# Optimization experiments

Hardware: AMD Instinct MI355X
Metric: run time of the kernel (lower is better)

## Reference

```python
import jax, jax.numpy as jnp
import numpy as np

B, T, C, H = 2, 2048, 1024, 16  # batch, seq, d_model, heads
D = C // H                       # head dim = 64


def setup_inputs() -> dict:
    key = jax.random.key(0)
    ks = jax.random.split(key, 5)
    s = 0.02  # init scale for weights
    return {
        "x": jax.random.normal(ks[0], (B, T, C), jnp.float32),
        "Wq": jax.random.normal(ks[1], (C, C), jnp.float32) * s,
        "bq": jnp.zeros((C,), jnp.float32),
        "Wk": jax.random.normal(ks[2], (C, C), jnp.float32) * s,
        "bk": jnp.zeros((C,), jnp.float32),
        "Wv": jax.random.normal(ks[3], (C, C), jnp.float32) * s,
        "bv": jnp.zeros((C,), jnp.float32),
        "Wo": jax.random.normal(ks[4], (C, C), jnp.float32) * s,
        "bo": jnp.zeros((C,), jnp.float32),
    }


def reference(x, Wq, bq, Wk, bk, Wv, bv, Wo, bo):
    b, t, c = x.shape
    h, d = H, C // H
    # QKV projections (torch Linear: x @ W.T + b), split into heads: b h t d
    q = (x @ Wq.T + bq).reshape(b, t, h, d).transpose(0, 2, 1, 3)
    k = (x @ Wk.T + bk).reshape(b, t, h, d).transpose(0, 2, 1, 3)
    v = (x @ Wv.T + bv).reshape(b, t, h, d).transpose(0, 2, 1, 3)

    scale = 1.0 / float(np.sqrt(d))
    att = jnp.einsum("bhqd,bhkd->bhqk", q, k) * scale  # [B,H,T,T]
    causal = jnp.tril(jnp.ones((t, t), dtype=bool))
    att = jnp.where(causal[None, None, :, :], att, -jnp.inf)
    att = jax.nn.softmax(att, axis=-1)
    att_weights = att  # attn_dropout with p=0 is identity

    y = jnp.einsum("bhqk,bhkd->bhqd", att, v)          # [B,H,T,D]
    y = y.transpose(0, 2, 1, 3).reshape(b, t, c)        # b q (h d)
    y = y @ Wo.T + bo                                   # out proj; resid_dropout p=0
    return y, att_weights
```

## Files before the change

kernel.cpp:

```cpp
#include <hip/hip_runtime.h>

#define DI __device__ __forceinline__

typedef __attribute__((ext_vector_type(8))) short short8;
typedef __attribute__((ext_vector_type(4))) float floatx4;
typedef unsigned short u16;

#define Bb 2
#define Tt 2048
#define Cc 1024
#define Hh 16
#define Dd 64
#define C1 0.1803368801111244f
#define NEGBIG (-1e30f)

DI float bf2f(u16 u) { union { unsigned int i; float f; } v; v.i = ((unsigned int)u) << 16; return v.f; }
DI u16 f2bf(float f) {
  union { float f; unsigned int i; } v; v.f = f;
  unsigned int i = v.i;
  unsigned int r = i + 0x7fffu + ((i >> 16) & 1u);
  return (u16)(r >> 16);
}

DI floatx4 mfma16(short8 a, short8 b, floatx4 c) {
  return __builtin_amdgcn_mfma_f32_16x16x32_bf16(a, b, c, 0, 0, 0);
}

DI void gload16(const u16* g, u16* l) {
  __builtin_amdgcn_global_load_lds(
      (const __attribute__((address_space(1))) unsigned int*)(g),
      (__attribute__((address_space(3))) unsigned int*)(l), 16, 0, 0);
}

DI uint4 load8(const void* p, size_t eoff, int isbf) {
  if (isbf) {
    return *(const uint4*)((const u16*)p + eoff);
  } else {
    const float* f = (const float*)p + eoff;
    float4 a = *(const float4*)f;
    float4 b = *(const float4*)(f + 4);
    union { uint4 u; u16 s[8]; } r;
    r.s[0] = f2bf(a.x); r.s[1] = f2bf(a.y); r.s[2] = f2bf(a.z); r.s[3] = f2bf(a.w);
    r.s[4] = f2bf(b.x); r.s[5] = f2bf(b.y); r.s[6] = f2bf(b.z); r.s[7] = f2bf(b.w);
    return r.u;
  }
}

DI float loadb(const void* p, int i, int isbf) {
  return isbf ? bf2f(((const u16*)p)[i]) : ((const float*)p)[i];
}

__global__ void detect_dtype(const u16* __restrict__ x, int* __restrict__ flag) {
  __shared__ int cnt[256];
  int c = 0;
  for (int i = threadIdx.x; i < 4096; i += 256) {
    unsigned u = x[2 * i];
    unsigned e = (u >> 7) & 0xFFu;
    c += (e == 0u || (e >= 100u && e <= 150u)) ? 1 : 0;
  }
  cnt[threadIdx.x] = c;
  __syncthreads();
  for (int s = 128; s > 0; s >>= 1) {
    if ((int)threadIdx.x < s) cnt[threadIdx.x] += cnt[threadIdx.x + s];
    __syncthreads();
  }
  if (threadIdx.x == 0) *flag = (cnt[0] > 2458) ? 1 : 0;
}

__global__ __launch_bounds__(256) void convert_all(
    const void* __restrict__ x,
    const void* __restrict__ wq, const void* __restrict__ wk,
    const void* __restrict__ wv, const void* __restrict__ wo,
    u16* __restrict__ xb,
    u16* __restrict__ wqb, u16* __restrict__ wkb,
    u16* __restrict__ wvb, u16* __restrict__ wob,
    const int* __restrict__ flagp) {
  const int isbf = *flagp;
  const void* src;
  u16* dst;
  size_t n;
  switch (blockIdx.y) {
    case 0: src = x;  dst = xb;  n = (size_t)Bb * Tt * Cc; break;
    case 1: src = wq; dst = wqb; n = (size_t)Cc * Cc; break;
    case 2: src = wk; dst = wkb; n = (size_t)Cc * Cc; break;
    case 3: src = wv; dst = wvb; n = (size_t)Cc * Cc; break;
    default: src = wo; dst = wob; n = (size_t)Cc * Cc; break;
  }
  size_t i8 = ((size_t)blockIdx.x * 256 + threadIdx.x) * 8;
  size_t step = (size_t)gridDim.x * 256 * 8;
  for (; i8 < n; i8 += step) {
    uint4 v = load8(src, i8, isbf);
    *(uint4*)(dst + i8) = v;
  }
}

__global__ __launch_bounds__(256) void qkv_gemm(
    const u16* __restrict__ Xb,
    const u16* __restrict__ Wqb, const u16* __restrict__ Wkb, const u16* __restrict__ Wvb,
    const void* __restrict__ bq, const void* __restrict__ bk, const void* __restrict__ bv,
    u16* __restrict__ Qb, u16* __restrict__ Kb, u16* __restrict__ Vb,
    const int* __restrict__ flagp) {
  __shared__ __align__(16) u16 As[128 * 32];
  __shared__ __align__(16) u16 Bs[128 * 32];
  const int isbf = *flagp;
  const int z = blockIdx.z;
  const u16* W = (z == 0) ? Wqb : (z == 1) ? Wkb : Wvb;
  const void* bias = (z == 0) ? bq : (z == 1) ? bk : bv;
  u16* Out = (z == 0) ? Qb : (z == 1) ? Kb : Vb;

  const int m0 = blockIdx.y * 128, n0 = blockIdx.x * 128;
  const int tid = threadIdx.x;
  const int w = tid >> 6, lane = tid & 63, quad = lane >> 4, l15 = lane & 15;
  const int wm = w >> 1, wn = w & 1;

  floatx4 acc[4][4];
#pragma unroll
  for (int a = 0; a < 4; ++a)
#pragma unroll
    for (int b2 = 0; b2 < 4; ++b2) acc[a][b2] = (floatx4){0.f, 0.f, 0.f, 0.f};

  const int s0 = w * 128 + lane, s1 = s0 + 64;
  const int rA0 = s0 >> 2, c0 = (s0 & 3) * 8;
  const int rA1 = s1 >> 2, c1 = (s1 & 3) * 8;
  const u16* gA0 = Xb + (size_t)(m0 + rA0) * Cc + c0;
  const u16* gA1 = Xb + (size_t)(m0 + rA1) * Cc + c1;
  const u16* gB0 = W + (size_t)(n0 + rA0) * Cc + c0;
  const u16* gB1 = W + (size_t)(n0 + rA1) * Cc + c1;
  u16* lA0 = As + w * 1024;
  u16* lA1 = As + w * 1024 + 512;
  u16* lB0 = Bs + w * 1024;
  u16* lB1 = Bs + w * 1024 + 512;

  for (int k0 = 0; k0 < Cc; k0 += 32) {
    __syncthreads();
    gload16(gA0 + k0, lA0);
    gload16(gA1 + k0, lA1);
    gload16(gB0 + k0, lB0);
    gload16(gB1 + k0, lB1);
    __syncthreads();
    short8 af[4], bfv[4];
#pragma unroll
    for (int t = 0; t < 4; ++t)
      af[t] = *(const short8*)(As + (wm * 64 + t * 16 + l15) * 32 + quad * 8);
#pragma unroll
    for (int t = 0; t < 4; ++t)
      bfv[t] = *(const short8*)(Bs + (wn * 64 + t * 16 + l15) * 32 + quad * 8);
#pragma unroll
    for (int tm = 0; tm < 4; ++tm)
#pragma unroll
      for (int tn = 0; tn < 4; ++tn) acc[tm][tn] = mfma16(af[tm], bfv[tn], acc[tm][tn]);
  }

  float bb[4];
#pragma unroll
  for (int tn = 0; tn < 4; ++tn) bb[tn] = loadb(bias, n0 + wn * 64 + tn * 16 + l15, isbf);
#pragma unroll
  for (int tm = 0; tm < 4; ++tm) {
#pragma unroll
    for (int tn = 0; tn < 4; ++tn) {
      int n = n0 + wn * 64 + tn * 16 + l15;
      int h = n >> 6, d = n & 63;
#pragma unroll
      for (int r = 0; r < 4; ++r) {
        int m = m0 + wm * 64 + tm * 16 + quad * 4 + r;
        int b = m >> 11, t = m & 2047;
        Out[(((size_t)(b * Hh + h) * Tt) + t) * Dd + d] = f2bf(acc[tm][tn][r] + bb[tn]);
      }
    }
  }
}

__global__ __launch_bounds__(256) void out_gemm(
    const u16* __restrict__ Y, const u16* __restrict__ Wob, const void* __restrict__ bo,
    float* __restrict__ Out, const int* __restrict__ flagp) {
  __shared__ __align__(16) u16 As[128 * 32];
  __shared__ __align__(16) u16 Bs[128 * 32];
  const int isbf = *flagp;
  const int m0 = blockIdx.y * 128, n0 = blockIdx.x * 128;
  const int tid = threadIdx.x;
  const int w = tid >> 6, lane = tid & 63, quad = lane >> 4, l15 = lane & 15;
  const int wm = w >> 1, wn = w & 1;

  floatx4 acc[4][4];
#pragma unroll
  for (int a = 0; a < 4; ++a)
#pragma unroll
    for (int b2 = 0; b2 < 4; ++b2) acc[a][b2] = (floatx4){0.f, 0.f, 0.f, 0.f};

  const int s0 = w * 128 + lane, s1 = s0 + 64;
  const int rA0 = s0 >> 2, c0 = (s0 & 3) * 8;
  const int rA1 = s1 >> 2, c1 = (s1 & 3) * 8;
  const u16* gA0 = Y + (size_t)(m0 + rA0) * Cc + c0;
  const u16* gA1 = Y + (size_t)(m0 + rA1) * Cc + c1;
  const u16* gB0 = Wob + (size_t)(n0 + rA0) * Cc + c0;
  const u16* gB1 = Wob + (size_t)(n0 + rA1) * Cc + c1;
  u16* lA0 = As + w * 1024;
  u16* lA1 = As + w * 1024 + 512;
  u16* lB0 = Bs + w * 1024;
  u16* lB1 = Bs + w * 1024 + 512;

  for (int k0 = 0; k0 < Cc; k0 += 32) {
    __syncthreads();
    gload16(gA0 + k0, lA0);
    gload16(gA1 + k0, lA1);
    gload16(gB0 + k0, lB0);
    gload16(gB1 + k0, lB1);
    __syncthreads();
    short8 af[4], bfv[4];
#pragma unroll
    for (int t = 0; t < 4; ++t)
      af[t] = *(const short8*)(As + (wm * 64 + t * 16 + l15) * 32 + quad * 8);
#pragma unroll
    for (int t = 0; t < 4; ++t)
      bfv[t] = *(const short8*)(Bs + (wn * 64 + t * 16 + l15) * 32 + quad * 8);
#pragma unroll
    for (int tm = 0; tm < 4; ++tm)
#pragma unroll
      for (int tn = 0; tn < 4; ++tn) acc[tm][tn] = mfma16(af[tm], bfv[tn], acc[tm][tn]);
  }

  float bb[4];
#pragma unroll
  for (int tn = 0; tn < 4; ++tn) bb[tn] = loadb(bo, n0 + wn * 64 + tn * 16 + l15, isbf);
#pragma unroll
  for (int tm = 0; tm < 4; ++tm)
#pragma unroll
    for (int tn = 0; tn < 4; ++tn) {
      int n = n0 + wn * 64 + tn * 16 + l15;
#pragma unroll
      for (int r = 0; r < 4; ++r) {
        int m = m0 + wm * 64 + tm * 16 + quad * 4 + r;
        Out[(size_t)m * Cc + n] = acc[tm][tn][r] + bb[tn];
      }
    }
}

__global__ __launch_bounds__(512) void attn_kernel(
    const u16* __restrict__ Qbuf, const u16* __restrict__ Kbuf, const u16* __restrict__ Vbuf,
    float* __restrict__ Att, u16* __restrict__ Ybuf) {
  __shared__ __align__(16) u16 Ks[128 * 72];
  __shared__ __align__(16) u16 Vts[64 * 136];
  __shared__ __align__(16) u16 Ps[8 * 16 * 40];

  const int id = blockIdx.x;
  const int qt = 15 - (id >> 5);
  const int hb = id & 31;
  const int b = hb >> 4, h = hb & 15;

  const int tid = threadIdx.x;
  const int w = tid >> 6, lane = tid & 63, quad = lane >> 4, l15 = lane & 15;

  const size_t headoff = (size_t)(b * Hh + h) * Tt * Dd;
  const u16* Qh = Qbuf + headoff;
  const u16* Kh = Kbuf + headoff;
  const u16* Vh = Vbuf + headoff;
  float* attO = Att + (size_t)(b * Hh + h) * Tt * Tt;
  u16* Psw = Ps + w * 640;

  const int q0 = qt * 128;
  const int qw = q0 + w * 16;

  const int vrow = tid >> 2, vcb = (tid & 3) * 16;

  short8 aq0 = *(const short8*)(Qh + (size_t)(qw + l15) * Dd + quad * 8);
  short8 aq1 = *(const short8*)(Qh + (size_t)(qw + l15) * Dd + 32 + quad * 8);

  float m4[4], l4[4];
#pragma unroll
  for (int r = 0; r < 4; ++r) { m4[r] = NEGBIG; l4[r] = 0.f; }

  for (int c = 0; c <= qt; ++c) {
    const int kb = c * 128;
    __syncthreads();
#pragma unroll
    for (int i = 0; i < 2; ++i) {
      int slot = tid + i * 512;
      int rr = slot >> 3, g = slot & 7;
      *(uint4*)(Ks + rr * 72 + g * 8) = *(const uint4*)(Kh + (size_t)(kb + rr) * Dd + g * 8);
    }
    __syncthreads();

    floatx4 s[8];
#pragma unroll
    for (int kt = 0; kt < 8; ++kt) {
      short8 b0 = *(const short8*)(Ks + (kt * 16 + l15) * 72 + quad * 8);
      short8 b1 = *(const short8*)(Ks + (kt * 16 + l15) * 72 + 32 + quad * 8);
      floatx4 t = (floatx4){0.f, 0.f, 0.f, 0.f};
      t = mfma16(aq0, b0, t);
      t = mfma16(aq1, b1, t);
      s[kt] = t;
    }
    const bool partial = (kb + 127 > qw);
#pragma unroll
    for (int r = 0; r < 4; ++r) {
      const int qi = qw + quad * 4 + r;
      float e[8];
      float bm = NEGBIG;
#pragma unroll
      for (int kt = 0; kt < 8; ++kt) {
        float s2 = s[kt][r] * C1;
        if (partial) {
          int key = kb + kt * 16 + l15;
          s2 = (key <= qi) ? s2 : NEGBIG;
        }
        e[kt] = s2;
        bm = fmaxf(bm, s2);
      }
      float mn = fmaxf(m4[r], bm);
      float sum = 0.f;
#pragma unroll
      for (int kt = 0; kt < 8; ++kt) sum += exp2f(e[kt] - mn);
      l4[r] = l4[r] * exp2f(m4[r] - mn) + sum;
      m4[r] = mn;
    }
  }
#pragma unroll
  for (int r = 0; r < 4; ++r) {
    float m = m4[r], l = l4[r];
#pragma unroll
    for (int off = 1; off <= 8; off <<= 1) {
      float mo = __shfl_xor(m, off, 64);
      float lo = __shfl_xor(l, off, 64);
      float mn = fmaxf(m, mo);
      l = l * exp2f(m - mn) + lo * exp2f(mo - mn);
      m = mn;
    }
    m4[r] = m; l4[r] = l;
  }
  float lrec[4];
#pragma unroll
  for (int r = 0; r < 4; ++r) lrec[r] = 1.0f / l4[r];

  floatx4 yacc[4];
#pragma unroll
  for (int dt = 0; dt < 4; ++dt) yacc[dt] = (floatx4){0.f, 0.f, 0.f, 0.f};

  uint4 va = *(const uint4*)(Vh + (size_t)vrow * Dd + vcb);
  uint4 vb = *(const uint4*)(Vh + (size_t)vrow * Dd + vcb + 8);

  for (int c = 0; c <= qt; ++c) {
    const int kb = c * 128;
    __syncthreads();
#pragma unroll
    for (int i = 0; i < 2; ++i) {
      int slot = tid + i * 512;
      int rr = slot >> 3, g = slot & 7;
      *(uint4*)(Ks + rr * 72 + g * 8) = *(const uint4*)(Kh + (size_t)(kb + rr) * Dd + g * 8);
    }
    {
      union { uint4 u; u16 sv[8]; } cv;
      cv.u = va;
#pragma unroll
      for (int j = 0; j < 8; ++j) Vts[(vcb + j) * 136 + vrow] = cv.sv[j];
      cv.u = vb;
#pragma unroll
      for (int j = 0; j < 8; ++j) Vts[(vcb + 8 + j) * 136 + vrow] = cv.sv[j];
    }
    if (c < qt) {
      va = *(const uint4*)(Vh + (size_t)(kb + 128 + vrow) * Dd + vcb);
      vb = *(const uint4*)(Vh + (size_t)(kb + 128 + vrow) * Dd + vcb + 8);
    }
    __syncthreads();

    floatx4 s[8];
#pragma unroll
    for (int kt = 0; kt < 8; ++kt) {
      short8 b0 = *(const short8*)(Ks + (kt * 16 + l15) * 72 + quad * 8);
      short8 b1 = *(const short8*)(Ks + (kt * 16 + l15) * 72 + 32 + quad * 8);
      floatx4 t = (floatx4){0.f, 0.f, 0.f, 0.f};
      t = mfma16(aq0, b0, t);
      t = mfma16(aq1, b1, t);
      s[kt] = t;
    }

    const bool partial = (kb + 127 > qw);
#pragma unroll
    for (int ks = 0; ks < 4; ++ks) {
#pragma unroll
      for (int kk = 0; kk < 2; ++kk) {
        const int kt = ks * 2 + kk;
#pragma unroll
        for (int r = 0; r < 4; ++r) {
          const int row = quad * 4 + r;
          const int qi = qw + row;
          const int key = kb + kt * 16 + l15;
          float p = exp2f(fminf(s[kt][r] * C1 - m4[r], 0.f)) * lrec[r];
          if (partial && key > qi) p = 0.f;
          attO[(size_t)qi * Tt + key] = p;
          Psw[row * 40 + kk * 16 + l15] = f2bf(p);
        }
      }
      short8 ap = *(const short8*)(Psw + l15 * 40 + quad * 8);
#pragma unroll
      for (int dt = 0; dt < 4; ++dt) {
        short8 bv = *(const short8*)(Vts + (dt * 16 + l15) * 136 + ks * 32 + quad * 8);
        yacc[dt] = mfma16(ap, bv, yacc[dt]);
      }
    }
  }

  {
    uint4 z; z.x = 0u; z.y = 0u; z.z = 0u; z.w = 0u;
    for (int c = qt + 1; c < 16; ++c) {
      const int kb = c * 128;
#pragma unroll
      for (int i = 0; i < 8; ++i) {
        int slot = tid + i * 512;
        int row = slot >> 5, g = slot & 31;
        *(uint4*)(attO + (size_t)(q0 + row) * Tt + kb + g * 4) = z;
      }
    }
  }

#pragma unroll
  for (int dt = 0; dt < 4; ++dt) {
#pragma unroll
    for (int r = 0; r < 4; ++r) {
      const int qi = qw + quad * 4 + r;
      Ybuf[(size_t)(b * Tt + qi) * Cc + h * Dd + dt * 16 + l15] = f2bf(yacc[dt][r]);
    }
  }
}

extern "C" void kernel_launch(void* const* d_in, const int* in_sizes, int n_in,
                              void* d_out, int out_size, void* d_ws, size_t ws_size,
                              hipStream_t stream) {
  const void* x  = d_in[0];
  const void* Wq = d_in[1];
  const void* bq = d_in[2];
  const void* Wk = d_in[3];
  const void* bk = d_in[4];
  const void* Wv = d_in[5];
  const void* bv = d_in[6];
  const void* Wo = d_in[7];
  const void* bo = d_in[8];
  float* out = (float*)d_out;

  const size_t NTC = (size_t)Bb * Tt * Cc;
  const size_t CC = (size_t)Cc * Cc;

  char* wsb = (char*)d_ws;
  int* flag = (int*)wsb;
  u16* Qb = (u16*)(wsb + 256);
  u16* Kb = Qb + NTC;
  u16* Vb = Kb + NTC;
  u16* Yb = Vb + NTC;
  u16* Xb = Yb + NTC;
  u16* Wqb = Xb + NTC;
  u16* Wkb = Wqb + CC;
  u16* Wvb = Wkb + CC;
  u16* Wob = Wvb + CC;

  hipLaunchKernelGGL(detect_dtype, dim3(1), dim3(256), 0, stream, (const u16*)x, flag);
  hipLaunchKernelGGL(convert_all, dim3(512, 5), dim3(256), 0, stream,
                     x, Wq, Wk, Wv, Wo, Xb, Wqb, Wkb, Wvb, Wob, flag);
  hipLaunchKernelGGL(qkv_gemm, dim3(8, 32, 3), dim3(256), 0, stream,
                     Xb, Wqb, Wkb, Wvb, bq, bk, bv, Qb, Kb, Vb, flag);
  float* attOut = out + NTC;
  hipLaunchKernelGGL(attn_kernel, dim3(512), dim3(512), 0, stream,
                     Qb, Kb, Vb, attOut, Yb);
  hipLaunchKernelGGL(out_gemm, dim3(8, 32, 1), dim3(256), 0, stream,
                     Yb, Wob, bo, out, flag);
}
```

Baseline: 706.5 us.

## Split attention into stats and PV kernels with smaller 64-row query tiles

Splits the fused two-pass attention kernel into two kernels. The first computes per-row softmax max and reciprocal sum into a workspace buffer. The second recomputes scores, writes the normalized attention probabilities and accumulates P·V. Query tiles shrink from 128 to 64 rows and blocks from 512 to 256 threads, doubling the grid for better load balance and occupancy. The cost is an extra launch, a small stats buffer round-trip, and partially wasted work on the diagonal key block, since 128-key chunks now cover 64-row tiles.

```diff
diff --git a/kernel.cpp b/kernel.cpp
--- a/kernel.cpp
+++ b/kernel.cpp
@@ -235,15 +235,13 @@
     }
 }
 
-__global__ __launch_bounds__(512) void attn_kernel(
-    const u16* __restrict__ Qbuf, const u16* __restrict__ Kbuf, const u16* __restrict__ Vbuf,
-    float* __restrict__ Att, u16* __restrict__ Ybuf) {
+__global__ __launch_bounds__(256) void attn_stats(
+    const u16* __restrict__ Qbuf, const u16* __restrict__ Kbuf,
+    float2* __restrict__ Sb) {
   __shared__ __align__(16) u16 Ks[128 * 72];
-  __shared__ __align__(16) u16 Vts[64 * 136];
-  __shared__ __align__(16) u16 Ps[8 * 16 * 40];
 
   const int id = blockIdx.x;
-  const int qt = 15 - (id >> 5);
+  const int qt = 31 - (id >> 5);
   const int hb = id & 31;
   const int b = hb >> 4, h = hb & 15;
 
@@ -253,14 +251,9 @@
   const size_t headoff = (size_t)(b * Hh + h) * Tt * Dd;
   const u16* Qh = Qbuf + headoff;
   const u16* Kh = Kbuf + headoff;
-  const u16* Vh = Vbuf + headoff;
-  float* attO = Att + (size_t)(b * Hh + h) * Tt * Tt;
-  u16* Psw = Ps + w * 640;
-
-  const int q0 = qt * 128;
+
+  const int q0 = qt * 64;
   const int qw = q0 + w * 16;
-
-  const int vrow = tid >> 2, vcb = (tid & 3) * 16;
 
   short8 aq0 = *(const short8*)(Qh + (size_t)(qw + l15) * Dd + quad * 8);
   short8 aq1 = *(const short8*)(Qh + (size_t)(qw + l15) * Dd + 32 + quad * 8);
@@ -269,12 +262,14 @@
 #pragma unroll
   for (int r = 0; r < 4; ++r) { m4[r] = NEGBIG; l4[r] = 0.f; }
 
-  for (int c = 0; c <= qt; ++c) {
+  const int nact = (qt >> 1) + 1;
+
+  for (int c = 0; c < nact; ++c) {
     const int kb = c * 128;
     __syncthreads();
 #pragma unroll
-    for (int i = 0; i < 2; ++i) {
-      int slot = tid + i * 512;
+    for (int i = 0; i < 4; ++i) {
+      int slot = tid + i * 256;
       int rr = slot >> 3, g = slot & 7;
       *(uint4*)(Ks + rr * 72 + g * 8) = *(const uint4*)(Kh + (size_t)(kb + rr) * Dd + g * 8);
     }
@@ -327,38 +322,94 @@
     }
     m4[r] = m; l4[r] = l;
   }
-  float lrec[4];
-#pragma unroll
-  for (int r = 0; r < 4; ++r) lrec[r] = 1.0f / l4[r];
+  if (l15 == 0) {
+#pragma unroll
+    for (int r = 0; r < 4; ++r) {
+      int qi = qw + quad * 4 + r;
+      float2 st; st.x = m4[r]; st.y = 1.0f / l4[r];
+      Sb[(size_t)(b * Hh + h) * Tt + qi] = st;
+    }
+  }
+}
+
+__global__ __launch_bounds__(256) void attn_pv(
+    const u16* __restrict__ Qbuf, const u16* __restrict__ Kbuf, const u16* __restrict__ Vbuf,
+    const float2* __restrict__ Sb,
+    float* __restrict__ Att, u16* __restrict__ Ybuf) {
+  __shared__ __align__(16) u16 Ks[128 * 72];
+  __shared__ __align__(16) u16 Vts[64 * 136];
+  __shared__ __align__(16) u16 Ps[4 * 16 * 40];
+
+  const int id = blockIdx.x;
+  const int qt = 31 - (id >> 5);
+  const int hb = id & 31;
+  const int b = hb >> 4, h = hb & 15;
+
+  const int tid = threadIdx.x;
+  const int w = tid >> 6, lane = tid & 63, quad = lane >> 4, l15 = lane & 15;
+
+  const size_t headoff = (size_t)(b * Hh + h) * Tt * Dd;
+  const u16* Qh = Qbuf + headoff;
+  const u16* Kh = Kbuf + headoff;
+  const u16* Vh = Vbuf + headoff;
+  float* attO = Att + (size_t)(b * Hh + h) * Tt * Tt;
+  u16* Psw = Ps + w * 640;
+
+  const int q0 = qt * 64;
+  const int qw = q0 + w * 16;
+
+  const int vrow = tid >> 1, vcb = (tid & 1) * 32;
+
+  short8 aq0 = *(const short8*)(Qh + (size_t)(qw + l15) * Dd + quad * 8);
+  short8 aq1 = *(const short8*)(Qh + (size_t)(qw + l15) * Dd + 32 + quad * 8);
+
+  float m4[4], lrec[4];
+#pragma unroll
+  for (int r = 0; r < 4; ++r) {
+    float2 st = Sb[(size_t)(b * Hh + h) * Tt + qw + quad * 4 + r];
+    m4[r] = st.x; lrec[r] = st.y;
+  }
 
   floatx4 yacc[4];
 #pragma unroll
   for (int dt = 0; dt < 4; ++dt) yacc[dt] = (floatx4){0.f, 0.f, 0.f, 0.f};
 
-  uint4 va = *(const uint4*)(Vh + (size_t)vrow * Dd + vcb);
-  uint4 vb = *(const uint4*)(Vh + (size_t)vrow * Dd + vcb + 8);
-
-  for (int c = 0; c <= qt; ++c) {
+  const int nact = (qt >> 1) + 1;
+
+  uint4 v0 = *(const uint4*)(Vh + (size_t)vrow * Dd + vcb);
+  uint4 v1 = *(const uint4*)(Vh + (size_t)vrow * Dd + vcb + 8);
+  uint4 v2 = *(const uint4*)(Vh + (size_t)vrow * Dd + vcb + 16);
+  uint4 v3 = *(const uint4*)(Vh + (size_t)vrow * Dd + vcb + 24);
+
+  for (int c = 0; c < nact; ++c) {
     const int kb = c * 128;
     __syncthreads();
 #pragma unroll
-    for (int i = 0; i < 2; ++i) {
-      int slot = tid + i * 512;
+    for (int i = 0; i < 4; ++i) {
+      int slot = tid + i * 256;
       int rr = slot >> 3, g = slot & 7;
       *(uint4*)(Ks + rr * 72 + g * 8) = *(const uint4*)(Kh + (size_t)(kb + rr) * Dd + g * 8);
     }
     {
       union { uint4 u; u16 sv[8]; } cv;
-      cv.u = va;
+      cv.u = v0;
 #pragma unroll
       for (int j = 0; j < 8; ++j) Vts[(vcb + j) * 136 + vrow] = cv.sv[j];
-      cv.u = vb;
+      cv.u = v1;
 #pragma unroll
       for (int j = 0; j < 8; ++j) Vts[(vcb + 8 + j) * 136 + vrow] = cv.sv[j];
-    }
-    if (c < qt) {
-      va = *(const uint4*)(Vh + (size_t)(kb + 128 + vrow) * Dd + vcb);
-      vb = *(const uint4*)(Vh + (size_t)(kb + 128 + vrow) * Dd + vcb + 8);
+      cv.u = v2;
+#pragma unroll
+      for (int j = 0; j < 8; ++j) Vts[(vcb + 16 + j) * 136 + vrow] = cv.sv[j];
+      cv.u = v3;
+#pragma unroll
+      for (int j = 0; j < 8; ++j) Vts[(vcb + 24 + j) * 136 + vrow] = cv.sv[j];
+    }
+    if (c + 1 < nact) {
+      v0 = *(const uint4*)(Vh + (size_t)(kb + 128 + vrow) * Dd + vcb);
+      v1 = *(const uint4*)(Vh + (size_t)(kb + 128 + vrow) * Dd + vcb + 8);
+      v2 = *(const uint4*)(Vh + (size_t)(kb + 128 + vrow) * Dd + vcb + 16);
+      v3 = *(const uint4*)(Vh + (size_t)(kb + 128 + vrow) * Dd + vcb + 24);
     }
     __syncthreads();
 
@@ -401,11 +452,11 @@
 
   {
     uint4 z; z.x = 0u; z.y = 0u; z.z = 0u; z.w = 0u;
-    for (int c = qt + 1; c < 16; ++c) {
+    for (int c = nact; c < 16; ++c) {
       const int kb = c * 128;
 #pragma unroll
       for (int i = 0; i < 8; ++i) {
-        int slot = tid + i * 512;
+        int slot = tid + i * 256;
         int row = slot >> 5, g = slot & 31;
         *(uint4*)(attO + (size_t)(q0 + row) * Tt + kb + g * 4) = z;
       }
@@ -450,6 +501,7 @@
   u16* Wkb = Wqb + CC;
   u16* Wvb = Wkb + CC;
   u16* Wob = Wvb + CC;
+  float2* Sb = (float2*)(Wob + CC);
 
   hipLaunchKernelGGL(detect_dtype, dim3(1), dim3(256), 0, stream, (const u16*)x, flag);
   hipLaunchKernelGGL(convert_all, dim3(512, 5), dim3(256), 0, stream,
@@ -457,8 +509,10 @@
   hipLaunchKernelGGL(qkv_gemm, dim3(8, 32, 3), dim3(256), 0, stream,
                      Xb, Wqb, Wkb, Wvb, bq, bk, bv, Qb, Kb, Vb, flag);
   float* attOut = out + NTC;
-  hipLaunchKernelGGL(attn_kernel, dim3(512), dim3(512), 0, stream,
-                     Qb, Kb, Vb, attOut, Yb);
+  hipLaunchKernelGGL(attn_stats, dim3(1024), dim3(256), 0, stream,
+                     Qb, Kb, Sb);
+  hipLaunchKernelGGL(attn_pv, dim3(1024), dim3(256), 0, stream,
+                     Qb, Kb, Vb, Sb, attOut, Yb);
   hipLaunchKernelGGL(out_gemm, dim3(8, 32, 1), dim3(256), 0, stream,
                      Yb, Wob, bo, out, flag);
 }
```

Result: slower. 738.2 us (+4.5%).
